# Performance work log

Hardware: AMD Instinct MI355X
Metric: run time of the kernel (lower is better)

## Reference

```python
import jax, jax.numpy as jnp
import numpy as np

N, E, B = 4096, 8192, 128


def seg_softmax(logits, seg, n):
    m = jax.ops.segment_max(logits, seg, num_segments=n)
    e = jnp.exp(logits - m[seg])
    s = jax.ops.segment_sum(e, seg, num_segments=n)
    return e / (s[seg] + 1e-16)


def gat(x, src, dst, W, a_src, a_dst, b, H, C, n):
    # PyG GATConv, concat=False (mean over heads), self-loops already appended
    h = (x @ W).reshape(n, H, C)
    al_s = jnp.sum(h * a_src, -1)  # [n,H]
    al_d = jnp.sum(h * a_dst, -1)
    logits = jax.nn.leaky_relu(al_s[src] + al_d[dst], 0.2)  # [E',H]
    alpha = seg_softmax(logits, dst, n)
    out = jax.ops.segment_sum(h[src] * alpha[:, :, None], dst, num_segments=n)
    return out.mean(1) + b


def gcn(x, src, dst, W, b, n):
    deg = jax.ops.segment_sum(jnp.ones_like(dst, jnp.float32), dst, num_segments=n)
    dis = jnp.where(deg > 0, deg ** -0.5, 0.0)
    norm = dis[src] * dis[dst]
    h = x @ W
    return jax.ops.segment_sum(h[src] * norm[:, None], dst, num_segments=n) + b


def transformer_conv(x, src, dst, Wq, bq, Wk, bk, Wv, bv, Ws, bs, H, C, n):
    # PyG TransformerConv, concat=False, root_weight=True, no self-loops
    q = (x @ Wq + bq).reshape(n, H, C)
    k = (x @ Wk + bk).reshape(n, H, C)
    v = (x @ Wv + bv).reshape(n, H, C)
    logits = jnp.sum(q[dst] * k[src], -1) / jnp.sqrt(jnp.float32(C))  # [E,H]
    alpha = seg_softmax(logits, dst, n)
    agg = jax.ops.segment_sum(v[src] * alpha[:, :, None], dst, num_segments=n)
    return agg.mean(1) + (x @ Ws + bs)


def gap(x, batch, nb):
    s = jax.ops.segment_sum(x, batch, num_segments=nb)
    cnt = jax.ops.segment_sum(jnp.ones(x.shape[0], x.dtype), batch, num_segments=nb)
    return s / jnp.maximum(cnt, 1.0)[:, None]


def setup_inputs() -> dict:
    key = jax.random.key(0)
    ks = iter(jax.random.split(key, 64))
    p = {}
    p['x'] = jax.random.normal(next(ks), (N, 78), jnp.float32)
    p['fp'] = (jax.random.uniform(next(ks), (B, 1489)) > 0.5).astype(jnp.float32)
    p['edge_index'] = jax.random.randint(next(ks), (2, E), 0, N, jnp.int32)
    p['batch'] = (jnp.arange(N, dtype=jnp.int32) // (N // B))
    def w(k, shp, fan):
        return jax.random.normal(k, shp, jnp.float32) * (1.0 / np.sqrt(fan))
    # GAT layers (in, out, heads=8)
    for name, ci, co in [('g1', 78, 2048), ('g2', 2048, 1024), ('g3', 1024, 512)]:
        p[name + '_w'] = w(next(ks), (ci, 8 * co), ci)
        p[name + '_as'] = w(next(ks), (8, co), co)
        p[name + '_ad'] = w(next(ks), (8, co), co)
        p[name + '_b'] = jnp.zeros((co,), jnp.float32)
    p['gcn_w'] = w(next(ks), (512, 256), 512)
    p['gcn_b'] = jnp.zeros((256,), jnp.float32)
    # TransformerConv 78->512, heads=4
    for nm in ['t_wq', 't_wk', 't_wv']:
        p[nm] = w(next(ks), (78, 4 * 512), 78)
    for nm in ['t_bq', 't_bk', 't_bv']:
        p[nm] = jnp.zeros((4 * 512,), jnp.float32)
    p['t_ws'] = w(next(ks), (78, 512), 78)
    p['t_bs'] = jnp.zeros((512,), jnp.float32)
    p['fc1_w'] = w(next(ks), (1489, 128), 1489); p['fc1_b'] = jnp.zeros((128,), jnp.float32)
    p['fc2_w'] = w(next(ks), (128, 256), 128); p['fc2_b'] = jnp.zeros((256,), jnp.float32)
    for nm, ci, co in [('b1', 1024, 256), ('b2', 256, 128), ('b3', 128, 64), ('b4', 64, 1)]:
        p[nm + '_w'] = w(next(ks), (ci, co), ci)
        p[nm + '_b'] = jnp.zeros((co,), jnp.float32)
    return p


def reference(x, fp, edge_index, batch,
              g1_w, g1_as, g1_ad, g1_b, g2_w, g2_as, g2_ad, g2_b,
              g3_w, g3_as, g3_ad, g3_b, gcn_w, gcn_b,
              t_wq, t_wk, t_wv, t_bq, t_bk, t_bv, t_ws, t_bs,
              fc1_w, fc1_b, fc2_w, fc2_b,
              b1_w, b1_b, b2_w, b2_b, b3_w, b3_b, b4_w, b4_b):
    n = x.shape[0]
    sl = jnp.arange(n, dtype=edge_index.dtype)
    src_sl = jnp.concatenate([edge_index[0], sl])  # with self loops (GAT/GCN)
    dst_sl = jnp.concatenate([edge_index[1], sl])
    h = jax.nn.relu(gat(x, src_sl, dst_sl, g1_w, g1_as, g1_ad, g1_b, 8, 2048, n))
    h = jax.nn.relu(gat(h, src_sl, dst_sl, g2_w, g2_as, g2_ad, g2_b, 8, 1024, n))
    h = jax.nn.relu(gat(h, src_sl, dst_sl, g3_w, g3_as, g3_ad, g3_b, 8, 512, n))
    h = gcn(h, src_sl, dst_sl, gcn_w, gcn_b, n)
    x_gat = gap(h, batch, B)  # [B,256]
    fpn = jax.nn.relu(fp @ fc1_w + fc1_b)
    fpn = jax.nn.relu(fpn @ fc2_w + fc2_b)  # [B,256]
    xt = jax.nn.relu(transformer_conv(x, edge_index[0], edge_index[1],
                                      t_wq, t_bq, t_wk, t_bk, t_wv, t_bv,
                                      t_ws, t_bs, 4, 512, n))
    x_trans = gap(xt, batch, B)  # [B,512]
    xc = jnp.concatenate([x_gat, x_trans, fpn], axis=1)  # [B,1024]
    h = jax.nn.relu(xc @ b1_w + b1_b)
    h = jax.nn.relu(h @ b2_w + b2_b)
    h = jax.nn.relu(h @ b3_w + b3_b)
    return jax.nn.sigmoid(h @ b4_w + b4_b)
```

## Files before the change

kernel.cpp:

```cpp
#include <hip/hip_runtime.h>

typedef unsigned short u16;
typedef unsigned int   u32;

typedef __bf16 bf16x8 __attribute__((ext_vector_type(8)));
typedef float  f32x4  __attribute__((ext_vector_type(4)));

#define NNODE 4096
#define NEDGE 8192
#define NEG   12288

__device__ __forceinline__ float blo(u32 u){ return __uint_as_float(u<<16); }
__device__ __forceinline__ float bhi(u32 u){ return __uint_as_float(u & 0xffff0000u); }
__device__ __forceinline__ u16 f2b(float f){
  u32 u = __float_as_uint(f);
  u += 0x7fffu + ((u>>16)&1u);
  return (u16)(u>>16);
}
__device__ __forceinline__ void split_bf(float a, u16& hi, u16& lo){
  u32 u = __float_as_uint(a);
  u32 r = u + 0x7fffu + ((u>>16)&1u);
  hi = (u16)(r>>16);
  float h = __uint_as_float(r & 0xffff0000u);
  float l = a - h;
  u32 u2 = __float_as_uint(l);
  lo = (u16)((u2 + 0x7fffu + ((u2>>16)&1u)) >> 16);
}
__device__ __forceinline__ u16 hi_bf(float a){
  u32 u = __float_as_uint(a);
  return (u16)((u + 0x7fffu + ((u>>16)&1u)) >> 16);
}

#define GL2LDS(g,l) __builtin_amdgcn_global_load_lds((const __attribute__((address_space(1))) unsigned int*)(g), (__attribute__((address_space(3))) unsigned int*)(l), 16, 0, 0)

__global__ __launch_bounds__(256) void zero_i(int* p, int n){
  int i = blockIdx.x*256 + threadIdx.x; if (i<n) p[i]=0;
}
__global__ __launch_bounds__(256) void hist_k(const int* __restrict__ ei, int* deg_g, int* deg_t){
  int e = blockIdx.x*256 + threadIdx.x; if (e>=NEG) return;
  int dv = (e<NEDGE) ? ei[NEDGE+e] : e-NEDGE;
  atomicAdd(&deg_g[dv],1);
  if (e<NEDGE) atomicAdd(&deg_t[dv],1);
}
__global__ __launch_bounds__(1024) void scan4096(const int* __restrict__ deg, int* __restrict__ off){
  __shared__ int lds[1024];
  int tid = threadIdx.x;
  int v[4]; int s=0;
  #pragma unroll
  for (int j=0;j<4;j++){ v[j]=deg[tid*4+j]; s+=v[j]; }
  lds[tid]=s; __syncthreads();
  for (int d=1; d<1024; d<<=1){
    int t = (tid>=d) ? lds[tid-d] : 0;
    __syncthreads();
    lds[tid] += t;
    __syncthreads();
  }
  int base = (tid>0) ? lds[tid-1] : 0;
  #pragma unroll
  for (int j=0;j<4;j++){ off[tid*4+j]=base; base+=v[j]; }
  if (tid==1023) off[4096]=base;
}
__global__ __launch_bounds__(256) void scatter_k(const int* __restrict__ ei,
    const int* __restrict__ off_g, int* cur_g, int* csr_g,
    const int* __restrict__ off_t, int* cur_t, int* csr_t){
  int e = blockIdx.x*256 + threadIdx.x; if (e>=NEG) return;
  int s, dv;
  if (e<NEDGE){ s=ei[e]; dv=ei[NEDGE+e]; } else { s=dv=e-NEDGE; }
  int p = atomicAdd(&cur_g[dv],1);
  csr_g[off_g[dv]+p]=s;
  if (e<NEDGE){ int p2 = atomicAdd(&cur_t[dv],1); csr_t[off_t[dv]+p2]=s; }
}
__global__ __launch_bounds__(256) void mkdis(const int* __restrict__ deg, float* dis){
  int i = blockIdx.x*256 + threadIdx.x; if (i>=NNODE) return;
  int d = deg[i]; dis[i] = d>0 ? rsqrtf((float)d) : 0.f;
}
__global__ __launch_bounds__(128) void pad_x(const float* __restrict__ x, float* __restrict__ xp,
                                             u16* __restrict__ xh){
  int n = blockIdx.x, c = threadIdx.x;
  if (c<96){
    float v = (c<78) ? x[(size_t)n*78+c] : 0.f;
    if (c<80) xp[(size_t)n*80+c] = v;
    xh[(size_t)n*96+c] = hi_bf(v);
  }
}
__global__ __launch_bounds__(256) void repack_w1(const float* __restrict__ g1w, float* __restrict__ w1r){
  int i = blockIdx.x*256 + threadIdx.x;
  int kk = i >> 11, c = i & 2047;
  int h = kk/80, k2 = kk - h*80;
  w1r[i] = (k2<78) ? g1w[(size_t)k2*16384 + h*2048 + c] : 0.f;
}

__global__ __launch_bounds__(256) void tpd(const float* __restrict__ in, int Ntot, int n0,
    int K, int Kp, u16* __restrict__ outh){
  __shared__ float t[32][33];
  int bx = blockIdx.x*32;
  int by = blockIdx.y*32;
  int tx = threadIdx.x & 31, ty = threadIdx.x >> 5;
  for (int i=ty;i<32;i+=8){
    int kk=by+i;
    t[i][tx] = (kk<K) ? in[(size_t)kk*Ntot + n0 + bx + tx] : 0.f;
  }
  __syncthreads();
  for (int i=ty;i<32;i+=8){
    int nn=bx+i, kk=by+tx;
    if (kk<Kp) outh[(size_t)nn*Kp+kk] = hi_bf(t[tx][i]);
  }
}

__global__ __launch_bounds__(256) void mk_wsT(const float* __restrict__ wsv, const float* __restrict__ wdv,
    u16* __restrict__ th, u16* __restrict__ tl, int Kp){
  int i = blockIdx.x*256 + threadIdx.x;
  if (i >= 16*Kp) return;
  int r = i / Kp, k = i - r*Kp;
  float v = (r<8) ? wsv[k*8+r] : wdv[k*8+(r-8)];
  u16 h,l; split_bf(v,h,l);
  th[i]=h; tl[i]=l;
}


template<int KS>
__global__ __launch_bounds__(256,4) void alk_mm(
    const u16* __restrict__ Ah, const u16* __restrict__ Al, int lda,
    const u16* __restrict__ Bh, const u16* __restrict__ Bl,
    float* __restrict__ alsd, int K)
{
  __shared__ __align__(16) u16 Ash[128*32], Asl[128*32], Bsh[16*32], Bsl[16*32];
  int tid = threadIdx.x, lane = tid & 63, wave = tid >> 6;
  int bm = blockIdx.y*128;
  int kb = blockIdx.x*(K/KS), ke = kb + K/KS;
  int m16 = lane & 15, quad = lane >> 4;
  int srow = lane >> 2;
  int skk = (((lane & 3) - (srow >> 1)) & 3) * 8;
  int kq  = (((quad + (m16 >> 1)) & 3)) * 8;
  f32x4 acc[2] = {};
  for (int k0=kb; k0<ke; k0+=32){
    __syncthreads();
    #pragma unroll
    for (int t=0;t<2;t++){
      int g = wave + t*4; int row = g*16 + srow;
      GL2LDS(Ah + (size_t)(bm+row)*lda + k0 + skk, &Ash[g*512]);
      GL2LDS(Al + (size_t)(bm+row)*lda + k0 + skk, &Asl[g*512]);
    }
    if (wave==0) GL2LDS(Bh + (size_t)srow*lda + k0 + skk, &Bsh[0]);
    if (wave==1) GL2LDS(Bl + (size_t)srow*lda + k0 + skk, &Bsl[0]);
    __syncthreads();
    bf16x8 bh = *(const bf16x8*)&Bsh[m16*32+kq];
    bf16x8 bl = *(const bf16x8*)&Bsl[m16*32+kq];
    #pragma unroll
    for (int i=0;i<2;i++){
      bf16x8 ah = *(const bf16x8*)&Ash[(wave*32+i*16+m16)*32+kq];
      bf16x8 al = *(const bf16x8*)&Asl[(wave*32+i*16+m16)*32+kq];
      acc[i] = __builtin_amdgcn_mfma_f32_16x16x32_bf16(ah, bh, acc[i],0,0,0);
      acc[i] = __builtin_amdgcn_mfma_f32_16x16x32_bf16(al, bh, acc[i],0,0,0);
      acc[i] = __builtin_amdgcn_mfma_f32_16x16x32_bf16(ah, bl, acc[i],0,0,0);
    }
  }
  #pragma unroll
  for (int i=0;i<2;i++){
    int row0 = bm + wave*32 + i*16 + quad*4;
    #pragma unroll
    for (int r=0;r<4;r++)
      atomicAdd(&alsd[(size_t)(row0+r)*16 + m16], acc[i][r]);
  }
}

#define BM 128
#define BN 128
template<int EPI, int SA, typename CT>
__global__ __launch_bounds__(256,4) void mgemm(
    const u16* __restrict__ Ah, const u16* __restrict__ Al, int lda,
    const u16* __restrict__ Bh, int ldb,
    CT* __restrict__ C, int ldc, int K,
    const float* __restrict__ bias, float scale,
    u16* __restrict__ Chi, u16* __restrict__ Clo)
{
  __shared__ __align__(16) u16 Ash[128*32];
  __shared__ __align__(16) u16 Bsh[128*32];
  __shared__ __align__(16) u16 Asl[SA?128*32:16];
  int tid = threadIdx.x;
  int bm = blockIdx.y*BM, bn = blockIdx.x*BN;
  int lane = tid & 63, wave = tid >> 6;
  int wr = (wave>>1)*64, wc = (wave&1)*64;
  int m16 = lane & 15, quad = lane >> 4;
  int srow = lane >> 2;
  int skk = (((lane & 3) - (srow >> 1)) & 3) * 8;
  int kq  = (((quad + (m16 >> 1)) & 3)) * 8;

  f32x4 acc[4][4] = {};
  for (int k0=0; k0<K; k0+=32){
    __syncthreads();
    #pragma unroll
    for (int t=0;t<2;t++){
      int g = wave + t*4;
      int row = g*16 + srow;
      GL2LDS(Ah + (size_t)(bm+row)*lda + k0 + skk, &Ash[g*512]);
      if (SA) GL2LDS(Al + (size_t)(bm+row)*lda + k0 + skk, &Asl[g*512]);
      GL2LDS(Bh + (size_t)(bn+row)*ldb + k0 + skk, &Bsh[g*512]);
    }
    __syncthreads();
    bf16x8 ah[4], al_[4], bh_[4];
    #pragma unroll
    for (int i=0;i<4;i++){
      ah[i]  = *(const bf16x8*)&Ash[(wr+i*16+m16)*32 + kq];
      if (SA) al_[i] = *(const bf16x8*)&Asl[(wr+i*16+m16)*32 + kq];
    }
    #pragma unroll
    for (int j=0;j<4;j++)
      bh_[j] = *(const bf16x8*)&Bsh[(wc+j*16+m16)*32 + kq];
    #pragma unroll
    for (int i=0;i<4;i++)
      #pragma unroll
      for (int j=0;j<4;j++){
        acc[i][j] = __builtin_amdgcn_mfma_f32_16x16x32_bf16(ah[i], bh_[j], acc[i][j], 0,0,0);
        if (SA) acc[i][j] = __builtin_amdgcn_mfma_f32_16x16x32_bf16(al_[i], bh_[j], acc[i][j], 0,0,0);
      }
  }
  #pragma unroll
  for (int i=0;i<4;i++){
    int row0 = bm + wr + i*16 + quad*4;
    #pragma unroll
    for (int j=0;j<4;j++){
      int col = bn + wc + j*16 + m16;
      float bv = (EPI==1||EPI==5) ? bias[col] : 0.f;
      #pragma unroll
      for (int r=0;r<4;r++){
        float v = acc[i][j][r];
        if constexpr (EPI==5){
          v = fmaxf(v*scale + bv, 0.f);
          size_t idx = (size_t)(row0+r)*ldc + col;
          u16 h_, l_; split_bf(v, h_, l_);
          Chi[idx]=h_; Clo[idx]=l_;
        } else {
          if (EPI==1) v += bv;
          size_t idx = (size_t)(row0+r)*ldc + col;
          if constexpr (sizeof(CT)==2) C[idx] = (CT)f2b(v);
          else C[idx] = (CT)v;
        }
      }
    }
  }
}

__device__ __forceinline__ void stA8(const u16* __restrict__ A, int lda, u16* dst,
                                     int bm, int kt, int h, int w, int lane){
  int q = ((lane&7) ^ (lane>>3)) * 8;
  #pragma unroll
  for (int t=0;t<2;t++){
    int rbase = t*128 + h*64 + w*8;
    int rl = rbase + (lane>>3);
    GL2LDS(A + (size_t)(bm+rl)*lda + kt*64 + q, dst + rbase*64);
  }
}
__device__ __forceinline__ void stB8(const u16* __restrict__ B, int ldb, u16* dst,
                                     int bn, int kt, int nh, int w, int lane){
  int q = ((lane&7) ^ (lane>>3)) * 8;
  #pragma unroll
  for (int t=0;t<2;t++){
    int rbase = (w>>1)*64 + nh*32 + (w&1)*16 + t*8;
    int rl = rbase + (lane>>3);
    GL2LDS(B + (size_t)(bn+rl)*ldb + kt*64 + q, dst + rbase*64);
  }
}
#define LDX8(BUF, ROW, KS) \
  (*(const bf16x8*)&(BUF)[(ROW)*64 + ((((KS)*4 + quad) ^ (m16 & 7)))*8])
#define RDA8(BUF, MH) \
  _Pragma("unroll") for (int mi=0;mi<4;mi++){ \
    a_[mi][0] = LDX8(BUF, wr*128 + ((MH)*4+mi)*16 + m16, 0); \
    a_[mi][1] = LDX8(BUF, wr*128 + ((MH)*4+mi)*16 + m16, 1); }
#define RDB8(BUF, NH, BB) \
  _Pragma("unroll") for (int nj=0;nj<2;nj++){ \
    BB[nj][0] = LDX8(BUF, wc*64 + ((NH)*2+nj)*16 + m16, 0); \
    BB[nj][1] = LDX8(BUF, wc*64 + ((NH)*2+nj)*16 + m16, 1); }
#define MMQ8(MH, NH, BB) \
  _Pragma("unroll") for (int mi=0;mi<4;mi++) \
    _Pragma("unroll") for (int nj=0;nj<2;nj++){ \
      acc[(MH)*4+mi][(NH)*2+nj] = __builtin_amdgcn_mfma_f32_16x16x32_bf16(a_[mi][0], BB[nj][0], acc[(MH)*4+mi][(NH)*2+nj],0,0,0); \
      acc[(MH)*4+mi][(NH)*2+nj] = __builtin_amdgcn_mfma_f32_16x16x32_bf16(a_[mi][1], BB[nj][1], acc[(MH)*4+mi][(NH)*2+nj],0,0,0); }
#define LGKM0 asm volatile("s_waitcnt lgkmcnt(0)" ::: "memory")
#define BAR   __builtin_amdgcn_s_barrier()
#define VM8   asm volatile("s_waitcnt vmcnt(8)" ::: "memory")
#define MMRUN(MH,NH,BB) \
  __builtin_amdgcn_s_setprio(1); MMQ8(MH,NH,BB); __builtin_amdgcn_s_setprio(0);

__global__ __launch_bounds__(512,2) void mgemm8(
    const u16* __restrict__ A, int lda,
    const u16* __restrict__ B, int ldb,
    u16* __restrict__ C, int ldc, int K, int nbx)
{
  __shared__ __align__(16) u16 As0[16384], As1[16384], Bs0[16384], Bs1[16384];
  int tid = threadIdx.x, lane = tid & 63, w = tid >> 6;
  int m16 = lane & 15, quad = lane >> 4;
  int wr = w >> 2, wc = w & 3;
  int nwg = (int)gridDim.x, bid = (int)blockIdx.x;
  int wg = (bid & 7)*(nwg>>3) + (bid>>3);
  int by = wg / nbx, bx = wg - by*nbx;
  int bm = by*256, bn = bx*256;
  int NT = K >> 6, NP = NT >> 1;
  f32x4 acc[8][4] = {};
  bf16x8 a_[4][2], b0_[2][2], b1_[2][2];
  stA8(A,lda,As0,bm,0,0,w,lane);
  stB8(B,ldb,Bs0,bn,0,0,w,lane);
  stB8(B,ldb,Bs0,bn,0,1,w,lane);
  stA8(A,lda,As0,bm,0,1,w,lane);
  stA8(A,lda,As1,bm,1,0,w,lane);
  stB8(B,ldb,Bs1,bn,1,0,w,lane);
  stB8(B,ldb,Bs1,bn,1,1,w,lane);
  stA8(A,lda,As1,bm,1,1,w,lane);
  VM8;
  BAR;
  for (int i=0;i<NP;i++){
    int t2 = 2*i+2; if (t2>NT-1) t2=NT-1;
    int t3 = 2*i+3; if (t3>NT-1) t3=NT-1;
    RDB8(Bs0,0,b0_);
    RDA8(As0,0);
    LGKM0; BAR;
    MMRUN(0,0,b0_);
    RDB8(Bs0,1,b1_);
    stA8(A,lda,As0,bm,t2,0,w,lane);
    stB8(B,ldb,Bs0,bn,t2,0,w,lane);
    LGKM0; BAR;
    MMRUN(0,1,b1_);
    RDA8(As0,1);
    stB8(B,ldb,Bs0,bn,t2,1,w,lane);
    LGKM0; BAR;
    MMRUN(1,1,b1_);
    stA8(A,lda,As0,bm,t2,1,w,lane);
    VM8; BAR;
    MMRUN(1,0,b0_);
    RDB8(Bs1,0,b0_);
    RDA8(As1,0);
    LGKM0; BAR;
    MMRUN(0,0,b0_);
    RDB8(Bs1,1,b1_);
    stA8(A,lda,As1,bm,t3,0,w,lane);
    stB8(B,ldb,Bs1,bn,t3,0,w,lane);
    LGKM0; BAR;
    MMRUN(0,1,b1_);
    RDA8(As1,1);
    stB8(B,ldb,Bs1,bn,t3,1,w,lane);
    LGKM0; BAR;
    MMRUN(1,1,b1_);
    stA8(A,lda,As1,bm,t3,1,w,lane);
    VM8; BAR;
    MMRUN(1,0,b0_);
  }
  asm volatile("s_waitcnt vmcnt(0)" ::: "memory");
  #pragma unroll
  for (int mi=0;mi<8;mi++){
    int row0 = bm + wr*128 + mi*16 + quad*4;
    #pragma unroll
    for (int nj=0;nj<4;nj++){
      int col = bn + wc*64 + nj*16 + m16;
      #pragma unroll
      for (int r=0;r<4;r++)
        C[(size_t)(row0+r)*ldc + col] = f2b(acc[mi][nj][r]);
    }
  }
}

__global__ __launch_bounds__(256) void wsvec(const float* __restrict__ W,
    const float* __restrict__ as_, const float* __restrict__ ad_,
    float* __restrict__ ws, float* __restrict__ wd,
    int Kreal, int H, int C)
{
  int wv = blockIdx.x*4 + (threadIdx.x>>6);
  int lane = threadIdx.x & 63;
  int k = wv / H, h = wv - k*H;
  float ps=0.f, pd=0.f;
  if (k < Kreal){
    const float* wr = W + (size_t)k*((size_t)H*C) + (size_t)h*C;
    const float* ar = as_ + (size_t)h*C;
    const float* dr = ad_ + (size_t)h*C;
    for (int c=lane;c<C;c+=64){ float w=wr[c]; ps += w*ar[c]; pd += w*dr[c]; }
  }
  #pragma unroll
  for (int o=32;o;o>>=1){ ps += __shfl_down(ps,o); pd += __shfl_down(pd,o); }
  if (lane==0){ ws[k*H+h]=ps; wd[k*H+h]=pd; }
}
__global__ __launch_bounds__(256) void alk(const float* __restrict__ X,
    const float* __restrict__ ws, const float* __restrict__ wd,
    float* __restrict__ alsd, int Kp)
{
  int n = blockIdx.x, tid = threadIdx.x;
  int hh = tid>>5, l32 = tid&31;
  const float* xr = X + (size_t)n*Kp;
  float ps=0.f, pd=0.f;
  for (int k=l32;k<Kp;k+=32){
    float xv = xr[k];
    ps += xv*ws[k*8+hh];
    pd += xv*wd[k*8+hh];
  }
  #pragma unroll
  for (int o=16;o;o>>=1){ ps += __shfl_down(ps,o,32); pd += __shfl_down(pd,o,32); }
  if (l32==0){ alsd[n*16+hh]=ps; alsd[n*16+8+hh]=pd; }
}

__global__ __launch_bounds__(256) void gat1_gather(
    const float* __restrict__ xpad, const float* __restrict__ alsd,
    const int* __restrict__ off, const int* __restrict__ csr,
    u16* __restrict__ y1h, u16* __restrict__ y1l)
{
  int d = blockIdx.x, tid = threadIdx.x;
  int hh = tid>>5, l32 = tid&31;
  int e0 = off[d], e1 = off[d+1];
  __shared__ float mh[8], lih[8], adh[8];
  __shared__ float wl[32][8];
  __shared__ int sl[32];
  if (tid < 8){
    float ad = alsd[d*16+8+tid]; adh[tid]=ad;
    float m=-1e30f, l=0.f;
    for (int e=e0;e<e1;++e){
      float xv = alsd[csr[e]*16+tid] + ad;
      xv = xv>0.f?xv:0.2f*xv;
      if (xv>m){ l = l*__expf(m-xv)+1.f; m=xv; } else l += __expf(xv-m);
    }
    mh[tid]=m; lih[tid]=1.f/l;
  }
  __syncthreads();
  float acc0=0.f, acc1=0.f, acc2v=0.f;
  for (int cb=e0; cb<e1; cb+=32){
    int ce = min(32, e1-cb);
    if (tid < ce*8){
      int j = tid>>3, h2 = tid&7;
      int s = csr[cb+j];
      if (h2==0) sl[j]=s;
      float xv = alsd[s*16+h2] + adh[h2];
      xv = xv>0.f?xv:0.2f*xv;
      wl[j][h2] = __expf(xv-mh[h2])*lih[h2];
    }
    __syncthreads();
    for (int j=0;j<ce;++j){
      float w = wl[j][hh];
      const float* xr = xpad + (size_t)sl[j]*80;
      acc0 += w*xr[l32];
      acc1 += w*xr[l32+32];
      if (l32 < 16) acc2v += w*xr[l32+64];
    }
    __syncthreads();
  }
  size_t base = (size_t)d*640 + hh*80;
  u16 h_, l_;
  split_bf(acc0, h_, l_); y1h[base+l32]=h_;    y1l[base+l32]=l_;
  split_bf(acc1, h_, l_); y1h[base+l32+32]=h_; y1l[base+l32+32]=l_;
  if (l32<16){ split_bf(acc2v, h_, l_); y1h[base+l32+64]=h_; y1l[base+l32+64]=l_; }
}

template<int HPC, int C>
__global__ __launch_bounds__(256) void gat_aggN(
    const u16* __restrict__ h, const float* __restrict__ alsd,
    const int* __restrict__ off, const int* __restrict__ csr,
    float* __restrict__ accum, int head0)
{
  constexpr int V = C/256;
  int d = blockIdx.x, tid = threadIdx.x;
  int e0=off[d], e1=off[d+1];
  __shared__ float mh[HPC], lih[HPC], adh[HPC];
  __shared__ float wl[32][HPC];
  __shared__ int sl[32];
  if (tid < HPC){
    float ad = alsd[d*16 + 8 + head0 + tid]; adh[tid]=ad;
    float m=-1e30f,l=0.f;
    for (int e=e0;e<e1;++e){
      float xv = alsd[csr[e]*16 + head0 + tid]+ad;
      xv = xv>0.f?xv:0.2f*xv;
      if (xv>m){ l=l*__expf(m-xv)+1.f; m=xv; } else l+=__expf(xv-m);
    }
    mh[tid]=m; lih[tid]=1.f/l;
  }
  __syncthreads();
  float acc[HPC][V];
  #pragma unroll
  for (int a=0;a<HPC;a++)
    #pragma unroll
    for (int v=0;v<V;v++) acc[a][v]=0.f;
  int c0 = tid*V;
  for (int cb=e0;cb<e1;cb+=32){
    int ce = min(32, e1-cb);
    if (tid < ce*HPC){
      int j = tid/HPC, h2 = tid - j*HPC;
      int s = csr[cb+j];
      if (h2==0) sl[j]=s;
      float xv = alsd[s*16 + head0 + h2] + adh[h2];
      xv = xv>0.f?xv:0.2f*xv;
      wl[j][h2] = __expf(xv-mh[h2])*lih[h2];
    }
    __syncthreads();
    for (int j=0;j<ce;++j){
      const u16* hr = h + (size_t)sl[j]*(HPC*C);
      #pragma unroll
      for (int a=0;a<HPC;a++){
        float w = wl[j][a];
        if constexpr (V==4){
          uint2 u = *(const uint2*)(hr + a*C + c0);
          acc[a][0] += w*blo(u.x); acc[a][1] += w*bhi(u.x);
          acc[a][2] += w*blo(u.y); acc[a][3] += w*bhi(u.y);
        } else {
          u32 u = *(const u32*)(hr + a*C + c0);
          acc[a][0] += w*blo(u); acc[a][1] += w*bhi(u);
        }
      }
    }
    __syncthreads();
  }
  float* ar = accum + (size_t)d*C + c0;
  #pragma unroll
  for (int v=0;v<V;v++){
    float s2 = 0.f;
    #pragma unroll
    for (int a=0;a<HPC;a++) s2 += acc[a][v];
    ar[v] += s2;
  }
}
__global__ __launch_bounds__(256) void finishx(const float* __restrict__ accum,
    const float* __restrict__ bias, float* __restrict__ xo, int Cmask){
  int i = blockIdx.x*256 + threadIdx.x;
  int c = i & Cmask;
  xo[i] = fmaxf(accum[i]*0.125f + bias[c], 0.f);
}
__global__ __launch_bounds__(256) void finishx2(const float* __restrict__ accum,
    const float* __restrict__ bias,
    u16* __restrict__ xh, u16* __restrict__ xl, int Cmask){
  int i = blockIdx.x*256 + threadIdx.x;
  int c = i & Cmask;
  float v = fmaxf(accum[i]*0.125f + bias[c], 0.f);
  u16 h_, l_; split_bf(v, h_, l_);
  xh[i]=h_; xl[i]=l_;
}

__global__ __launch_bounds__(256) void pool_gcn(const float* __restrict__ x3,
    const float* __restrict__ dis, const int* __restrict__ off, const int* __restrict__ csr,
    float* __restrict__ z)
{
  int g = blockIdx.x, tid = threadIdx.x;
  int c0 = tid*2;
  float a0=0.f, a1=0.f;
  for (int dd=0; dd<32; ++dd){
    int d = g*32+dd;
    int e0=off[d], e1=off[d+1];
    float b0=0.f, b1=0.f;
    for (int e=e0;e<e1;++e){
      int s = csr[e]; float ds = dis[s];
      const float* xr = x3 + (size_t)s*512 + c0;
      b0 += ds*xr[0]; b1 += ds*xr[1];
    }
    float dw = dis[d];
    a0 += dw*b0; a1 += dw*b1;
  }
  z[(size_t)g*512+c0]   = a0*(1.f/32.f);
  z[(size_t)g*512+c0+1] = a1*(1.f/32.f);
}

__global__ __launch_bounds__(256) void tr_agg(
  const u16* __restrict__ qkvs, const int* __restrict__ off, const int* __restrict__ csr,
  float* __restrict__ xt)
{
  int d = blockIdx.x, tid = threadIdx.x;
  int wv = tid>>6, lane = tid&63;
  int e0=off[d], e1=off[d+1];
  __shared__ float osum[4][512];
  __shared__ float sp[4][64];
  float qf[8];
  { uint4 u = *(const uint4*)(qkvs + (size_t)d*6656 + wv*512 + lane*8);
    qf[0]=blo(u.x); qf[1]=bhi(u.x); qf[2]=blo(u.y); qf[3]=bhi(u.y);
    qf[4]=blo(u.z); qf[5]=bhi(u.z); qf[6]=blo(u.w); qf[7]=bhi(u.w); }
  const float scale = 0.04419417382415922f;
  float m=-1e30f,l=0.f;
  for (int e=e0;e<e1;++e){
    int s = csr[e];
    uint4 u = *(const uint4*)(qkvs + (size_t)s*6656 + 2048 + wv*512 + lane*8);
    float p = qf[0]*blo(u.x)+qf[1]*bhi(u.x)+qf[2]*blo(u.y)+qf[3]*bhi(u.y)
            + qf[4]*blo(u.z)+qf[5]*bhi(u.z)+qf[6]*blo(u.w)+qf[7]*bhi(u.w);
    #pragma unroll
    for (int o=32;o;o>>=1) p += __shfl_xor(p,o);
    p *= scale;
    int idx = e-e0;
    if (lane==0 && idx<64) sp[wv][idx]=p;
    if (p>m){ l=l*__expf(m-p)+1.f; m=p; } else l+=__expf(p-m);
  }
  float li = (e1>e0)?1.f/l:0.f;
  float acc[8]={0.f,0.f,0.f,0.f,0.f,0.f,0.f,0.f};
  for (int e=e0;e<e1;++e){
    int s = csr[e];
    int idx = e-e0;
    float p;
    if (idx<64) p = sp[wv][idx];
    else {
      uint4 u = *(const uint4*)(qkvs + (size_t)s*6656 + 2048 + wv*512 + lane*8);
      p = qf[0]*blo(u.x)+qf[1]*bhi(u.x)+qf[2]*blo(u.y)+qf[3]*bhi(u.y)
        + qf[4]*blo(u.z)+qf[5]*bhi(u.z)+qf[6]*blo(u.w)+qf[7]*bhi(u.w);
      #pragma unroll
      for (int o=32;o;o>>=1) p += __shfl_xor(p,o);
      p *= scale;
    }
    float w = __expf(p - m)*li;
    uint4 u = *(const uint4*)(qkvs + (size_t)s*6656 + 4096 + wv*512 + lane*8);
    acc[0]+=w*blo(u.x); acc[1]+=w*bhi(u.x); acc[2]+=w*blo(u.y); acc[3]+=w*bhi(u.y);
    acc[4]+=w*blo(u.z); acc[5]+=w*bhi(u.z); acc[6]+=w*blo(u.w); acc[7]+=w*bhi(u.w);
  }
  #pragma unroll
  for (int j=0;j<8;j++) osum[wv][lane*8+j]=acc[j];
  __syncthreads();
  for (int c=tid;c<512;c+=256){
    u16 sk = qkvs[(size_t)d*6656 + 6144 + c];
    float o = (osum[0][c]+osum[1][c]+osum[2][c]+osum[3][c])*0.25f + blo((u32)sk);
    xt[(size_t)d*512+c] = fmaxf(o,0.f);
  }
}

__global__ __launch_bounds__(256) void catb(const float* __restrict__ bq, const float* __restrict__ bk,
    const float* __restrict__ bv, const float* __restrict__ bs, float* __restrict__ o){
  int i = blockIdx.x*256 + threadIdx.x; if (i>=6656) return;
  float v;
  if (i<2048) v=bq[i]; else if (i<4096) v=bk[i-2048];
  else if (i<6144) v=bv[i-4096]; else v=bs[i-6144];
  o[i]=v;
}

__device__ __forceinline__ float dotb(const u16* __restrict__ w, const float* __restrict__ s,
                                      int k0, int k1){
  float acc=0.f;
  #pragma unroll 4
  for (int k=k0;k<k1;k+=8){
    uint4 u = *(const uint4*)(w+k);
    float4 s0 = *(const float4*)(s+k);
    float4 s1 = *(const float4*)(s+k+4);
    acc += blo(u.x)*s0.x + bhi(u.x)*s0.y + blo(u.y)*s0.z + bhi(u.y)*s0.w
         + blo(u.z)*s1.x + bhi(u.z)*s1.y + blo(u.w)*s1.z + bhi(u.w)*s1.w;
  }
  return acc;
}
__global__ __launch_bounds__(256) void head_k(
  const float* __restrict__ z, const float* __restrict__ xt, const float* __restrict__ fp,
  const u16* __restrict__ gcnT, const float* __restrict__ gcn_b,
  const u16* __restrict__ fc1T, const float* __restrict__ fc1_b,
  const u16* __restrict__ fc2T, const float* __restrict__ fc2_b,
  const u16* __restrict__ b1T, const float* __restrict__ b1_b,
  const u16* __restrict__ b2T, const float* __restrict__ b2_b,
  const u16* __restrict__ b3T, const float* __restrict__ b3_b,
  const float* __restrict__ b4_w, const float* __restrict__ b4_b,
  float* __restrict__ out)
{
  int g = blockIdx.x, tid = threadIdx.x;
  __shared__ __align__(16) float xc[1024];
  __shared__ __align__(16) float sa[1504];
  __shared__ __align__(16) float sb[256];
  __shared__ __align__(16) float scm[256];
  for (int c=tid;c<512;c+=256) sa[c] = z[(size_t)g*512+c];
  __syncthreads();
  float vgcn = gcn_b[tid] + dotb(gcnT + (size_t)tid*512, sa, 0, 512);
  for (int c=tid;c<512;c+=256){
    float s=0.f;
    for (int i=0;i<32;i++) s += xt[(size_t)(g*32+i)*512 + c];
    xc[256+c] = s*(1.f/32.f);
  }
  xc[tid] = vgcn;
  __syncthreads();
  for (int c=tid;c<1496;c+=256) sa[c] = (c<1489) ? fp[(size_t)g*1489+c] : 0.f;
  __syncthreads();
  { int n = tid & 127, half = tid >> 7;
    sb[tid] = dotb(fc1T + (size_t)n*1496, sa, half?752:0, half?1496:752); }
  __syncthreads();
  if (tid<128) scm[tid] = fmaxf(sb[tid]+sb[tid+128]+fc1_b[tid], 0.f);
  __syncthreads();
  xc[768+tid] = fmaxf(fc2_b[tid] + dotb(fc2T + (size_t)tid*128, scm, 0, 128), 0.f);
  __syncthreads();
  sa[tid] = fmaxf(b1_b[tid] + dotb(b1T + (size_t)tid*1024, xc, 0, 1024), 0.f);
  __syncthreads();
  { int n = tid & 127, half = tid >> 7;
    sb[tid] = dotb(b2T + (size_t)n*256, sa, half*128, half*128+128); }
  __syncthreads();
  if (tid<128) scm[tid] = fmaxf(sb[tid]+sb[tid+128]+b2_b[tid], 0.f);
  __syncthreads();
  { int n = tid & 63, part = tid >> 6;
    sb[tid] = dotb(b3T + (size_t)n*128, scm, part*32, part*32+32); }
  __syncthreads();
  if (tid<64) sa[tid] = fmaxf(sb[tid]+sb[tid+64]+sb[tid+128]+sb[tid+192]+b3_b[tid], 0.f);
  __syncthreads();
  if (tid<64){
    float p = sa[tid]*b4_w[tid];
    #pragma unroll
    for (int o=32;o;o>>=1) p += __shfl_down(p,o);
    if (tid==0) out[g] = 1.f/(1.f+__expf(-(p + b4_b[0])));
  }
}

extern "C" void kernel_launch(void* const* d_in, const int* in_sizes, int n_in,
                              void* d_out, int out_size, void* d_ws, size_t ws_size,
                              hipStream_t stream)
{
  (void)in_sizes; (void)n_in; (void)out_size; (void)ws_size;
  const float* x     = (const float*)d_in[0];
  const float* fp    = (const float*)d_in[1];
  const int*   ei    = (const int*)d_in[2];
  const float* g1_w  = (const float*)d_in[4];
  const float* g1_as = (const float*)d_in[5];
  const float* g1_ad = (const float*)d_in[6];
  const float* g1_b  = (const float*)d_in[7];
  const float* g2_w  = (const float*)d_in[8];
  const float* g2_as = (const float*)d_in[9];
  const float* g2_ad = (const float*)d_in[10];
  const float* g2_b  = (const float*)d_in[11];
  const float* g3_w  = (const float*)d_in[12];
  const float* g3_as = (const float*)d_in[13];
  const float* g3_ad = (const float*)d_in[14];
  const float* g3_b  = (const float*)d_in[15];
  const float* gcn_w = (const float*)d_in[16];
  const float* gcn_b = (const float*)d_in[17];
  const float* t_wq  = (const float*)d_in[18];
  const float* t_wk  = (const float*)d_in[19];
  const float* t_wv  = (const float*)d_in[20];
  const float* t_bq  = (const float*)d_in[21];
  const float* t_bk  = (const float*)d_in[22];
  const float* t_bv  = (const float*)d_in[23];
  const float* t_ws  = (const float*)d_in[24];
  const float* t_bs  = (const float*)d_in[25];
  const float* fc1_w = (const float*)d_in[26];
  const float* fc1_b = (const float*)d_in[27];
  const float* fc2_w = (const float*)d_in[28];
  const float* fc2_b = (const float*)d_in[29];
  const float* b1_w  = (const float*)d_in[30];
  const float* b1_b  = (const float*)d_in[31];
  const float* b2_w  = (const float*)d_in[32];
  const float* b2_b  = (const float*)d_in[33];
  const float* b3_w  = (const float*)d_in[34];
  const float* b3_b  = (const float*)d_in[35];
  const float* b4_w  = (const float*)d_in[36];
  const float* b4_b  = (const float*)d_in[37];

  char* base = (char*)d_ws;
  size_t offb = 0;
  auto alloc = [&](size_t bytes)->void*{
    void* p = base + offb; offb = (offb + bytes + 255) & ~(size_t)255; return p;
  };
  int*   cnt   = (int*)alloc(16384*4);
  int*   off_g = (int*)alloc(4097*4);
  int*   off_t = (int*)alloc(4097*4);
  int*   csr_g = (int*)alloc(12288*4);
  int*   csr_t = (int*)alloc(8192*4);
  float* dis   = (float*)alloc(4096*4);
  float* xpad  = (float*)alloc((size_t)4096*80*4);
  u16*   xph   = (u16*)alloc((size_t)4096*96*2);
  float* alsd  = (float*)alloc((size_t)4096*16*4);
  float* wsv   = (float*)alloc((size_t)2048*8*4);
  float* wdv   = (float*)alloc((size_t)2048*8*4);
  u16*   wsTh  = (u16*)alloc((size_t)16*2048*2);
  u16*   wsTl  = (u16*)alloc((size_t)16*2048*2);
  float* zbuf  = (float*)alloc((size_t)128*512*4);
  float* cbias = (float*)alloc((size_t)6656*4);
  float* w1r   = (float*)alloc((size_t)640*2048*4);
  u16*   gcnT  = (u16*)alloc((size_t)256*512*2);
  u16*   fc1T  = (u16*)alloc((size_t)128*1496*2);
  u16*   fc2T  = (u16*)alloc((size_t)256*128*2);
  u16*   b1T   = (u16*)alloc((size_t)256*1024*2);
  u16*   b2T   = (u16*)alloc((size_t)128*256*2);
  u16*   b3T   = (u16*)alloc((size_t)64*128*2);
  char*  big   = (char*)alloc((size_t)140<<20);

  u16*   y1h   = (u16*)  (big);
  u16*   y1l   = (u16*)  (big + ((size_t)5<<20));
  u16*   w1rth = (u16*)  (big + ((size_t)10<<20));
  u16*   x1h   = (u16*)  (big + ((size_t)16<<20));
  u16*   x1l   = (u16*)  (big + ((size_t)32<<20));
  u16*   w2th  = (u16*)  (big + ((size_t)48<<20));
  u16*   h2    = (u16*)  (big + ((size_t)64<<20));
  float* acc2  = (float*)(big + ((size_t)96<<20));
  u16*   x2h   = (u16*)  (big + ((size_t)112<<20));
  u16*   x2l   = (u16*)  (big + ((size_t)120<<20));
  u16*   w3th  = (u16*)  (big);
  u16*   h3    = (u16*)  (big + ((size_t)8<<20));
  float* acc3  = (float*)(big + ((size_t)40<<20));
  float* x3    = (float*)(big + ((size_t)48<<20));
  u16*   qkvTh = (u16*)  (big);
  u16*   qkvs  = (u16*)  (big + ((size_t)8<<20));
  float* xt    = (float*)(big + ((size_t)64<<20));

  int* deg_g = cnt;       int* cur_g = cnt+4096;
  int* deg_t = cnt+8192;  int* cur_t = cnt+12288;

  zero_i<<<64,256,0,stream>>>(cnt, 16384);
  hist_k<<<48,256,0,stream>>>(ei, deg_g, deg_t);
  scan4096<<<1,1024,0,stream>>>(deg_g, off_g);
  scan4096<<<1,1024,0,stream>>>(deg_t, off_t);
  scatter_k<<<48,256,0,stream>>>(ei, off_g, cur_g, csr_g, off_t, cur_t, csr_t);
  mkdis<<<16,256,0,stream>>>(deg_g, dis);
  pad_x<<<4096,128,0,stream>>>(x, xpad, xph);
  repack_w1<<<5120,256,0,stream>>>(g1_w, w1r);
  tpd<<<dim3(8,16),256,0,stream>>>(gcn_w, 256, 0, 512, 512, gcnT);
  tpd<<<dim3(4,47),256,0,stream>>>(fc1_w, 128, 0, 1489, 1496, fc1T);
  tpd<<<dim3(8,4), 256,0,stream>>>(fc2_w, 256, 0, 128, 128, fc2T);
  tpd<<<dim3(8,32),256,0,stream>>>(b1_w,  256, 0, 1024, 1024, b1T);
  tpd<<<dim3(4,8), 256,0,stream>>>(b2_w,  128, 0, 256, 256, b2T);
  tpd<<<dim3(2,4), 256,0,stream>>>(b3_w,  64,  0, 128, 128, b3T);

  wsvec<<<160,256,0,stream>>>(g1_w, g1_as, g1_ad, wsv, wdv, 78, 8, 2048);
  alk<<<4096,256,0,stream>>>(xpad, wsv, wdv, alsd, 80);
  gat1_gather<<<4096,256,0,stream>>>(xpad, alsd, off_g, csr_g, y1h, y1l);
  tpd<<<dim3(64,20),256,0,stream>>>(w1r, 2048, 0, 640, 640, w1rth);
  mgemm<5,1,float><<<dim3(16,32),256,0,stream>>>(y1h, y1l, 640, w1rth, 640,
                                         nullptr, 2048, 640, g1_b, 0.125f, x1h, x1l);

  wsvec<<<4096,256,0,stream>>>(g2_w, g2_as, g2_ad, wsv, wdv, 2048, 8, 1024);
  mk_wsT<<<128,256,0,stream>>>(wsv, wdv, wsTh, wsTl, 2048);
  hipMemsetAsync(alsd, 0, (size_t)4096*16*4, stream);
  alk_mm<8><<<dim3(8,32),256,0,stream>>>(x1h, x1l, 2048, wsTh, wsTl, alsd, 2048);
  hipMemsetAsync(acc2, 0, (size_t)4096*1024*4, stream);
  for (int c=0;c<2;c++){
    tpd<<<dim3(128,64),256,0,stream>>>(g2_w, 8192, c*4096, 2048, 2048, w2th);
    mgemm8<<<256,512,0,stream>>>(x1h, 2048, w2th, 2048, h2, 4096, 2048, 16);
    gat_aggN<4,1024><<<4096,256,0,stream>>>(h2, alsd, off_g, csr_g, acc2, c*4);
  }
  finishx2<<<16384,256,0,stream>>>(acc2, g2_b, x2h, x2l, 1023);

  wsvec<<<2048,256,0,stream>>>(g3_w, g3_as, g3_ad, wsv, wdv, 1024, 8, 512);
  mk_wsT<<<64,256,0,stream>>>(wsv, wdv, wsTh, wsTl, 1024);
  hipMemsetAsync(alsd, 0, (size_t)4096*16*4, stream);
  alk_mm<8><<<dim3(8,32),256,0,stream>>>(x2h, x2l, 1024, wsTh, wsTl, alsd, 1024);
  hipMemsetAsync(acc3, 0, (size_t)4096*512*4, stream);
  tpd<<<dim3(128,32),256,0,stream>>>(g3_w, 4096, 0, 1024, 1024, w3th);
  mgemm8<<<256,512,0,stream>>>(x2h, 1024, w3th, 1024, h3, 4096, 1024, 16);
  gat_aggN<8,512><<<4096,256,0,stream>>>(h3, alsd, off_g, csr_g, acc3, 0);
  finishx<<<8192,256,0,stream>>>(acc3, g3_b, x3, 511);
  pool_gcn<<<128,256,0,stream>>>(x3, dis, off_g, csr_g, zbuf);

  tpd<<<dim3(64,3),256,0,stream>>>(t_wq, 2048, 0, 78, 96, qkvTh);
  tpd<<<dim3(64,3),256,0,stream>>>(t_wk, 2048, 0, 78, 96, qkvTh + (size_t)2048*96);
  tpd<<<dim3(64,3),256,0,stream>>>(t_wv, 2048, 0, 78, 96, qkvTh + (size_t)4096*96);
  tpd<<<dim3(16,3),256,0,stream>>>(t_ws, 512,  0, 78, 96, qkvTh + (size_t)6144*96);
  catb<<<26,256,0,stream>>>(t_bq, t_bk, t_bv, t_bs, cbias);
  mgemm<1,0,u16><<<dim3(52,32),256,0,stream>>>(xph, nullptr, 96, qkvTh, 96,
                                         qkvs, 6656, 96, cbias, 0.f, nullptr, nullptr);
  tr_agg<<<4096,256,0,stream>>>(qkvs, off_t, csr_t, xt);

  head_k<<<128,256,0,stream>>>(zbuf, xt, fp, gcnT, gcn_b,
                               fc1T, fc1_b, fc2T, fc2_b,
                               b1T, b1_b, b2T, b2_b, b3T, b3_b, b4_w, b4_b,
                               (float*)d_out);
}
```

Before: 754.9 us.

## Reschedule GEMM main loop with finer barriers and shifted global-to-LDS prefetch

Reworks the software pipeline in the bf16 MFMA GEMM. The last A sub-tile load of each stage is deferred into the next iteration, vmcnt waits drop from 8 to 6, and a partial lgkmcnt(8) wait comes before the barrier. Extra barriers now bracket each MFMA cluster so global loads and LDS reads interleave more evenly with matrix math. The goal is to hide memory latency better, at the cost of more barriers and a more fragile ordering of waits.

Result: slower. 770.7 us (+2.1%).

```diff
diff --git a/kernel.cpp b/kernel.cpp
--- a/kernel.cpp
+++ b/kernel.cpp
@@ -277,8 +277,9 @@
       acc[(MH)*4+mi][(NH)*2+nj] = __builtin_amdgcn_mfma_f32_16x16x32_bf16(a_[mi][0], BB[nj][0], acc[(MH)*4+mi][(NH)*2+nj],0,0,0); \
       acc[(MH)*4+mi][(NH)*2+nj] = __builtin_amdgcn_mfma_f32_16x16x32_bf16(a_[mi][1], BB[nj][1], acc[(MH)*4+mi][(NH)*2+nj],0,0,0); }
 #define LGKM0 asm volatile("s_waitcnt lgkmcnt(0)" ::: "memory")
+#define LGKM8 asm volatile("s_waitcnt lgkmcnt(8)" ::: "memory")
 #define BAR   __builtin_amdgcn_s_barrier()
-#define VM8   asm volatile("s_waitcnt vmcnt(8)" ::: "memory")
+#define VM6   asm volatile("s_waitcnt vmcnt(6)" ::: "memory")
 #define MMRUN(MH,NH,BB) \
   __builtin_amdgcn_s_setprio(1); MMQ8(MH,NH,BB); __builtin_amdgcn_s_setprio(0);
 
@@ -305,44 +306,56 @@
   stA8(A,lda,As1,bm,1,0,w,lane);
   stB8(B,ldb,Bs1,bn,1,0,w,lane);
   stB8(B,ldb,Bs1,bn,1,1,w,lane);
-  stA8(A,lda,As1,bm,1,1,w,lane);
-  VM8;
+  VM6;
   BAR;
   for (int i=0;i<NP;i++){
     int t2 = 2*i+2; if (t2>NT-1) t2=NT-1;
     int t3 = 2*i+3; if (t3>NT-1) t3=NT-1;
+    int t1n = 2*i+1;
     RDB8(Bs0,0,b0_);
     RDA8(As0,0);
-    LGKM0; BAR;
+    stA8(A,lda,As1,bm,t1n,1,w,lane);
+    LGKM8;
+    BAR; LGKM0;
     MMRUN(0,0,b0_);
+    BAR;
     RDB8(Bs0,1,b1_);
     stA8(A,lda,As0,bm,t2,0,w,lane);
+    BAR; LGKM0;
+    MMRUN(0,1,b1_);
+    BAR;
+    RDA8(As0,1);
     stB8(B,ldb,Bs0,bn,t2,0,w,lane);
-    LGKM0; BAR;
-    MMRUN(0,1,b1_);
-    RDA8(As0,1);
+    BAR; LGKM0;
+    MMRUN(1,1,b1_);
+    BAR;
     stB8(B,ldb,Bs0,bn,t2,1,w,lane);
-    LGKM0; BAR;
-    MMRUN(1,1,b1_);
-    stA8(A,lda,As0,bm,t2,1,w,lane);
-    VM8; BAR;
+    BAR;
     MMRUN(1,0,b0_);
+    VM6;
+    BAR;
     RDB8(Bs1,0,b0_);
     RDA8(As1,0);
-    LGKM0; BAR;
+    stA8(A,lda,As0,bm,t2,1,w,lane);
+    LGKM8;
+    BAR; LGKM0;
     MMRUN(0,0,b0_);
+    BAR;
     RDB8(Bs1,1,b1_);
     stA8(A,lda,As1,bm,t3,0,w,lane);
+    BAR; LGKM0;
+    MMRUN(0,1,b1_);
+    BAR;
+    RDA8(As1,1);
     stB8(B,ldb,Bs1,bn,t3,0,w,lane);
-    LGKM0; BAR;
-    MMRUN(0,1,b1_);
-    RDA8(As1,1);
+    BAR; LGKM0;
+    MMRUN(1,1,b1_);
+    BAR;
     stB8(B,ldb,Bs1,bn,t3,1,w,lane);
-    LGKM0; BAR;
-    MMRUN(1,1,b1_);
-    stA8(A,lda,As1,bm,t3,1,w,lane);
-    VM8; BAR;
+    BAR;
     MMRUN(1,0,b0_);
+    VM6;
+    BAR;
   }
   asm volatile("s_waitcnt vmcnt(0)" ::: "memory");
   #pragma unroll
```
